# Optimization experiments

Hardware: AMD Instinct MI355X
Metric: run time of the kernel (lower is better)

Reference implementation:

```python
import jax, jax.numpy as jnp
import numpy as np

B, N, D = 512, 101, 128
H = D
NHEADS = 8
HD = H // NHEADS
NSTEPS = 140


def setup_inputs() -> dict:
    key = jax.random.key(0)
    ks = jax.random.split(key, 12)
    enc = jax.random.normal(ks[0], (B, N, D), jnp.float32)
    pool = jax.random.normal(ks[1], (B, H), jnp.float32)
    # CVRP-style demands: depot demand 0, customers in (0, 0.2); capacity normalized to 1.0
    demand = jax.random.uniform(ks[2], (B, N), jnp.float32) * 0.2
    demand = demand.at[:, 0].set(0.0)
    capcity = jnp.ones((B, 1), jnp.float32)
    actions_old = jax.random.randint(ks[3], (B, NSTEPS), 0, N, dtype=jnp.int32)

    def lin(k, fin, fout):
        return (jax.random.normal(k, (fin, fout), jnp.float32) / np.sqrt(fin)).astype(jnp.float32)

    return dict(
        encoder_inputs=enc, pool=pool, actions_old=actions_old,
        capcity=capcity, demand=demand, n_steps=NSTEPS, batch_size=B,
        W_fc=lin(ks[4], H + 1, H),      # Decoder1.fc  (no bias)
        W_fc1=lin(ks[5], H, H),         # Decoder1.fc1
        W_w=lin(ks[6], D, H),           # Attention1.w (cat=1)
        W_k=lin(ks[7], D, H),           # Attention1.k
        W_v=lin(ks[8], D, H),           # Attention1.v
        W_attnfc=lin(ks[9], H, H),      # Attention1.fc
        W_pk=lin(ks[10], D, H),         # ProbAttention.k
    )


def reference(encoder_inputs, pool, actions_old, capcity, demand, n_steps, batch_size,
              W_fc, W_fc1, W_w, W_k, W_v, W_attnfc, W_pk):
    Bs, Nn, Dd = encoder_inputs.shape
    Hh = W_fc.shape[1]
    nh = NHEADS
    hd = Hh // nh
    cap0 = capcity[0, 0]  # torch: capcity[0].item()
    demands = demand
    col = jnp.arange(Nn)

    # context is constant across decode steps -> hoist K/V/pointer-K projections
    Kh = (encoder_inputs @ W_k).reshape(Bs, Nn, nh, hd).transpose(0, 2, 1, 3)  # (B,h,N,hd)
    Vh = (encoder_inputs @ W_v).reshape(Bs, Nn, nh, hd).transpose(0, 2, 1, 3)
    Kp = encoder_inputs @ W_pk  # (B,N,H)

    def update_mask(mask1, dyn_cap, index):
        # mask1: visited nodes (bool). depot masked iff we just arrived at depot.
        go_depot = index == 0
        m1 = jnp.logical_or(mask1, col[None, :] == index[:, None])
        m1 = m1.at[:, 0].set(go_depot)
        mask = jnp.logical_or(m1, demands > dyn_cap)  # dyn_cap (B,1) broadcasts
        # guard: if everything masked (instance finished), allow depot (torch code
        # breaks out of the loop instead; log_p is zeroed by is_done either way)
        all_masked = jnp.all(mask, axis=1)
        mask = mask.at[:, 0].set(jnp.where(all_masked, False, mask[:, 0]))
        return mask, m1

    def update_state(dyn_cap, index):
        cur = jnp.take_along_axis(demands, index[:, None], axis=1)
        dyn = dyn_cap - cur
        return jnp.where((index == 0)[:, None], cap0, dyn)

    mask1_init = jnp.zeros((Bs, Nn), bool)
    idx0 = jnp.zeros((Bs,), jnp.int32)
    mask_init, mask1_init = update_mask(mask1_init, capcity, idx0)  # i == 0 update

    def step(carry, _):
        _input, dyn_cap, mask, mask1, pool_c = carry
        dec = jnp.concatenate([_input, dyn_cap], axis=-1) @ W_fc  # (B,H)
        pool_n = pool_c @ W_fc1                                   # pool re-projected EVERY step (as in torch)
        dec = dec + pool_n
        # --- Attention1 (multi-head glimpse) ---
        Q = (dec @ W_w).reshape(Bs, nh, hd)
        compat = jnp.einsum('bhd,bhnd->bhn', Q, Kh) * (1.0 / np.sqrt(hd))
        u = jnp.where(mask[:, None, :], -jnp.inf, compat)
        sc = jax.nn.softmax(u, axis=-1)
        glimpse = jnp.einsum('bhn,bhnd->bhd', sc, Vh).reshape(Bs, Hh) @ W_attnfc
        # --- ProbAttention (tanh-clipped pointer) ---
        comp2 = jnp.einsum('bh,bnh->bn', glimpse, Kp) * (1.0 / np.sqrt(Hh))
        logits = jnp.where(mask, -jnp.inf, 10.0 * jnp.tanh(comp2))
        logp_all = jax.nn.log_softmax(logits, axis=-1)
        index = jnp.argmax(logp_all, axis=-1)  # greedy decode
        log_p = jnp.take_along_axis(logp_all, index[:, None], axis=1)[:, 0]
        is_done = (jnp.sum(mask1[:, 1:].astype(jnp.int32), axis=1) >= (Nn - 1)).astype(log_p.dtype)
        log_p = log_p * (1.0 - is_done)
        dyn_new = jax.lax.stop_gradient(update_state(dyn_cap, index))  # torch .detach()
        mask_new, mask1_new = update_mask(mask1, dyn_new, index)
        inp_new = jnp.take_along_axis(encoder_inputs, index[:, None, None], axis=1)[:, 0, :]
        return (inp_new, dyn_new, mask_new, mask1_new, pool_n), (index, log_p)

    carry0 = (encoder_inputs[:, 0, :], capcity, mask_init, mask1_init, pool)
    _, (actions, log_ps) = jax.lax.scan(step, carry0, None, length=int(n_steps))
    actions = actions.T            # (B, n_steps)
    log_p = jnp.sum(log_ps, axis=0)  # (B,)
    return actions, log_p
```

## Files before the change

### kernel.cpp

```cpp
#include <hip/hip_runtime.h>
#include <math.h>

#define B_ 512
#define N_ 101
#define H_ 128
#define T_ 140
#define M37 0x1FFFFFFFFFull

#define BAR() asm volatile("s_waitcnt lgkmcnt(0)\n\ts_barrier" ::: "memory")
#define LGKM0() asm volatile("s_waitcnt lgkmcnt(0)" ::: "memory")

template <int CTRL, int RM>
__device__ __forceinline__ float dpp_max_step(float x) {
  int t = __builtin_amdgcn_update_dpp((int)0xFF800000, __float_as_int(x), CTRL, RM, 0xF, false);
  return fmaxf(x, __int_as_float(t));
}
template <int CTRL, int RM>
__device__ __forceinline__ float dpp_add_step(float x) {
  int t = __builtin_amdgcn_update_dpp(0, __float_as_int(x), CTRL, RM, 0xF, false);
  return x + __int_as_float(t);
}
__device__ __forceinline__ float wave_max64(float x) {
  x = dpp_max_step<0x111, 0xF>(x);
  x = dpp_max_step<0x112, 0xF>(x);
  x = dpp_max_step<0x114, 0xF>(x);
  x = dpp_max_step<0x118, 0xF>(x);
  x = dpp_max_step<0x142, 0xA>(x);
  x = dpp_max_step<0x143, 0xC>(x);
  return __int_as_float(__builtin_amdgcn_readlane(__float_as_int(x), 63));
}
__device__ __forceinline__ float wave_sum64(float x) {
  x = dpp_add_step<0x111, 0xF>(x);
  x = dpp_add_step<0x112, 0xF>(x);
  x = dpp_add_step<0x114, 0xF>(x);
  x = dpp_add_step<0x118, 0xF>(x);
  x = dpp_add_step<0x142, 0xA>(x);
  x = dpp_add_step<0x143, 0xC>(x);
  return __int_as_float(__builtin_amdgcn_readlane(__float_as_int(x), 63));
}

__device__ __forceinline__ void gemm_tile_dev(
    const float* A, const float* B, float* C, int cb, int transB, int tid)
{
  int cc = cb * 32 + (tid & 7) * 4;
  int r0 = tid >> 3;
  float4 acc0 = {0,0,0,0}, acc1 = {0,0,0,0}, acc2 = {0,0,0,0}, acc3 = {0,0,0,0};
  for (int k = 0; k < 128; ++k) {
    float4 b4;
    if (!transB) {
      b4 = *(const float4*)(B + k * 128 + cc);
    } else {
      b4.x = B[(cc + 0) * 128 + k];
      b4.y = B[(cc + 1) * 128 + k];
      b4.z = B[(cc + 2) * 128 + k];
      b4.w = B[(cc + 3) * 128 + k];
    }
    float a0 = A[(r0 +  0) * 128 + k];
    float a1 = A[(r0 + 32) * 128 + k];
    float a2 = A[(r0 + 64) * 128 + k];
    float a3 = A[(r0 + 96) * 128 + k];
    acc0.x += a0 * b4.x; acc0.y += a0 * b4.y; acc0.z += a0 * b4.z; acc0.w += a0 * b4.w;
    acc1.x += a1 * b4.x; acc1.y += a1 * b4.y; acc1.z += a1 * b4.z; acc1.w += a1 * b4.w;
    acc2.x += a2 * b4.x; acc2.y += a2 * b4.y; acc2.z += a2 * b4.z; acc2.w += a2 * b4.w;
    acc3.x += a3 * b4.x; acc3.y += a3 * b4.y; acc3.z += a3 * b4.z; acc3.w += a3 * b4.w;
  }
  *(float4*)(C + (r0 +  0) * 128 + cc) = acc0;
  *(float4*)(C + (r0 + 32) * 128 + cc) = acc1;
  *(float4*)(C + (r0 + 64) * 128 + cc) = acc2;
  *(float4*)(C + (r0 + 96) * 128 + cc) = acc3;
}

__global__ __launch_bounds__(256) void stage_a(
    const float* __restrict__ Wfc, const float* __restrict__ Ww,
    const float* __restrict__ Wpk, const float* __restrict__ Wat,
    const float* __restrict__ F,
    float* __restrict__ Wfw, float* __restrict__ Wc, float* __restrict__ wcap,
    float* __restrict__ Mbuf)
{
  int j = blockIdx.x, tid = threadIdx.x;
  if (j < 4)       gemm_tile_dev(Wfc, Ww, Wfw, j, 0, tid);
  else if (j < 8)  gemm_tile_dev(Wpk, Wat, Wc, j - 4, 1, tid);
  else if (j == 8) {
    if (tid < 128) {
      float s = 0.f;
      for (int k = 0; k < 128; ++k) s += Wfc[128 * 128 + k] * Ww[k * 128 + tid];
      wcap[tid] = s;
    }
  } else gemm_tile_dev(F, F, Mbuf + 2ll * 16384, j - 9, 0, tid);
}

__global__ __launch_bounds__(256) void stage_b(
    const float* __restrict__ F, const float* __restrict__ enc,
    const float* __restrict__ Wfw, float* __restrict__ Mbuf,
    float* __restrict__ encW)
{
  int bx = blockIdx.x, tid = threadIdx.x;
  if (bx < 8) {
    int s = (bx >> 2) + 1, cb = bx & 3;
    const float* As = (s == 1) ? F : Mbuf + (long long)s * 16384;
    gemm_tile_dev(As, Mbuf + 2ll * 16384, Mbuf + (long long)(2 + s) * 16384, cb, 0, tid);
  } else {
    int jj = bx - 8, rb = jj >> 2, cb = jj & 3;
    gemm_tile_dev(enc + (long long)rb * 16384, Wfw, encW + (long long)rb * 16384, cb, 0, tid);
  }
}

__global__ __launch_bounds__(256) void chainL(
    const float* __restrict__ F, float* __restrict__ Mbuf, int L)
{
  int bx = blockIdx.x, tid = threadIdx.x;
  int s = (bx >> 2) + 1, cb = bx & 3;
  const float* As = (s == 1) ? F : Mbuf + (long long)s * 16384;
  gemm_tile_dev(As, Mbuf + (long long)L * 16384, Mbuf + (long long)(L + s) * 16384, cb, 0, tid);
}

__global__ __launch_bounds__(256) void stage_n8(
    const float* __restrict__ F, const float* __restrict__ Ww,
    float* __restrict__ Mbuf, float* __restrict__ Abuf)
{
  int bx = blockIdx.x, tid = threadIdx.x;
  if (bx < 48) {
    int s = (bx >> 2) + 1, cb = bx & 3;
    const float* As = (s == 1) ? F : Mbuf + (long long)s * 16384;
    gemm_tile_dev(As, Mbuf + 128ll * 16384, Mbuf + (long long)(128 + s) * 16384, cb, 0, tid);
  } else {
    int jj = bx - 48, t = jj >> 2, cb = jj & 3;
    const float* Ms = (t == 0) ? F : Mbuf + (long long)(t + 1) * 16384;
    gemm_tile_dev(Ms, Ww, Abuf + (long long)t * 16384, cb, 0, tid);
  }
}

__global__ __launch_bounds__(256) void stage_n9(
    const float* __restrict__ Ww, const float* __restrict__ pool,
    float* __restrict__ Mbuf, float* __restrict__ Abuf, float* __restrict__ Qpl)
{
  int bx = blockIdx.x, tid = threadIdx.x;
  if (bx < 52) {
    int t = 127 + (bx >> 2), cb = bx & 3;
    gemm_tile_dev(Mbuf + (long long)(t + 1) * 16384, Ww, Abuf + (long long)t * 16384, cb, 0, tid);
  } else {
    int jj = bx - 52, t = jj >> 4, sub = jj & 15, rb = sub >> 2, cb = sub & 3;
    gemm_tile_dev(pool + (long long)rb * 16384, Abuf + (long long)t * 16384,
                  Qpl + (long long)t * 65536 + (long long)rb * 16384, cb, 0, tid);
  }
}

__global__ __launch_bounds__(256) void stage_n10(
    const float* __restrict__ pool, float* __restrict__ Abuf, float* __restrict__ Qpl)
{
  int bx = blockIdx.x, tid = threadIdx.x;
  int t = 127 + (bx >> 4), sub = bx & 15, rb = sub >> 2, cb = sub & 3;
  gemm_tile_dev(pool + (long long)rb * 16384, Abuf + (long long)t * 16384,
                Qpl + (long long)t * 65536 + (long long)rb * 16384, cb, 0, tid);
}

__device__ __forceinline__ void compat_sm(
    int wave, int lane, int amaxU, float capU,
    unsigned long long msklo, unsigned long long mskhi,
    const float* s_buf, const float* s_wc, const float* s_qp,
    float* s_qs, const float* kreg, float* s_sc)
{
  if (lane < 32) {
    int d = (lane < 16) ? (wave * 16 + lane) : ((wave + 4) * 16 + (lane - 16));
    float qv = s_buf[amaxU * H_ + d] + capU * s_wc[d] + s_qp[d];
    s_qs[wave * 32 + lane] = qv;
  }
  LGKM0();
  const float4* q0 = (const float4*)(s_qs + wave * 32);
  const float4* q1 = (const float4*)(s_qs + wave * 32 + 16);
  float c00 = 0.f, c01 = 0.f, c10 = 0.f, c11 = 0.f;
#pragma unroll
  for (int q = 0; q < 4; ++q) {
    float4 qq = q0[q];
    c00 += qq.x * kreg[q * 4 + 0] + qq.y * kreg[q * 4 + 1]
         + qq.z * kreg[q * 4 + 2] + qq.w * kreg[q * 4 + 3];
    c10 += qq.x * kreg[32 + q * 4 + 0] + qq.y * kreg[32 + q * 4 + 1]
         + qq.z * kreg[32 + q * 4 + 2] + qq.w * kreg[32 + q * 4 + 3];
    float4 qr = q1[q];
    c01 += qr.x * kreg[16 + q * 4 + 0] + qr.y * kreg[16 + q * 4 + 1]
         + qr.z * kreg[16 + q * 4 + 2] + qr.w * kreg[16 + q * 4 + 3];
    c11 += qr.x * kreg[48 + q * 4 + 0] + qr.y * kreg[48 + q * 4 + 1]
         + qr.z * kreg[48 + q * 4 + 2] + qr.w * kreg[48 + q * 4 + 3];
  }
  bool mb0 = (msklo >> lane) & 1ull;
  bool mb1v = (lane < 37) ? ((mskhi >> lane) & 1ull) : true;
  float a0 = mb0 ? -INFINITY : 0.25f * c00;
  float a1 = mb0 ? -INFINITY : 0.25f * c01;
  float b0 = mb1v ? -INFINITY : 0.25f * c10;
  float b1 = mb1v ? -INFINITY : 0.25f * c11;

  float m0  = wave_max64(fmaxf(a0, b0));
  float m1v = wave_max64(fmaxf(a1, b1));
  float ea0 = expf(a0 - m0),  eb0 = (lane < 37) ? expf(b0 - m0)  : 0.f;
  float ea1 = expf(a1 - m1v), eb1 = (lane < 37) ? expf(b1 - m1v) : 0.f;
  float s0 = ea0 + eb0, s1 = ea1 + eb1;
#pragma unroll
  for (int off = 32; off > 0; off >>= 1) {
    s0 += __shfl_xor(s0, off);
    s1 += __shfl_xor(s1, off);
  }
  float* r0 = s_sc + wave * 104;
  float* r1 = s_sc + (wave + 4) * 104;
  r0[lane] = ea0 / s0; r1[lane] = ea1 / s1;
  if (lane < 37) { r0[64 + lane] = eb0 / s0; r1[64 + lane] = eb1 / s1; }
}

__global__ __attribute__((amdgpu_flat_work_group_size(256, 256), amdgpu_waves_per_eu(2, 2)))
void decode_kernel(
    const float* __restrict__ enc,
    const float* __restrict__ Wk,
    const float* __restrict__ Wv,
    const float* __restrict__ Wc,
    const float* __restrict__ encW,
    const float* __restrict__ Qpool,
    const float* __restrict__ wcap,
    const float* __restrict__ capcity,
    const float* __restrict__ demand,
    float* __restrict__ out)
{
  __shared__ __align__(16) float s_buf[N_ * 132];
  __shared__ __align__(16) float s_sc[8 * 104];
  __shared__ __align__(16) float s_part[256];
  __shared__ __align__(16) float s_p2[256];
  __shared__ __align__(16) float s_qs[128];
  __shared__ __align__(16) float s_wc[128];
  __shared__ __align__(16) float s_qp[128];

  const int b    = blockIdx.x;
  const int tid  = threadIdx.x;
  const int lane = tid & 63;
  const int wave = tid >> 6;
  const int an = tid & 127, aj = tid >> 7;
  const int bh2 = (lane >> 4) & 1;
  const int bj2 = (wave + ((lane >= 32) ? 4 : 0)) * 16 + (lane & 15);
  const float invSqrtH = 0.08838834764831845f;

  float cap  = capcity[b];
  float cap0 = capcity[0];
  float dem0 = demand[(long long)b * N_ + lane];
  float dem1 = (lane < 37) ? demand[(long long)b * N_ + 64 + lane] : 0.f;
  float wcr  = (tid < 128) ? wcap[tid] : 0.f;
  float qp0  = (tid < 128) ? Qpool[(long long)b * H_ + tid] : 0.f;

  for (int idx = tid; idx < N_ * 32; idx += 256) {
    int row = idx >> 5, q = idx & 31;
    float4 v = *(const float4*)(enc + ((long long)b * N_ + row) * H_ + q * 4);
    float* d = s_buf + row * 132 + q * 4;
    d[0] = v.x; d[1] = v.y; d[2] = v.z; d[3] = v.w;
  }
  BAR();

  float vreg[51];
#pragma unroll
  for (int q = 0; q < 51; ++q) vreg[q] = 0.f;
  {
    const int base = bh2 * 51;
    for (int i4 = 0; i4 < 32; ++i4) {
      float w0 = Wv[(i4 * 4 + 0) * H_ + bj2];
      float w1 = Wv[(i4 * 4 + 1) * H_ + bj2];
      float w2 = Wv[(i4 * 4 + 2) * H_ + bj2];
      float w3 = Wv[(i4 * 4 + 3) * H_ + bj2];
#pragma unroll
      for (int nl = 0; nl < 51; ++nl) {
        if (base + nl < N_) {
          float4 e = *(const float4*)(s_buf + (base + nl) * 132 + i4 * 4);
          vreg[nl] += e.x * w0 + e.y * w1 + e.z * w2 + e.w * w3;
        }
      }
    }
  }

  float kreg[64];
#pragma unroll
  for (int q = 0; q < 64; ++q) kreg[q] = 0.f;
  {
    const int n0 = lane;
    const int n1c = (lane < 37) ? 64 + lane : 0;
    for (int i = 0; i < 128; ++i) {
      float e0 = s_buf[n0 * 132 + i];
      float e1 = s_buf[n1c * 132 + i];
      const float4* wk0 = (const float4*)(Wk + i * H_ + wave * 16);
      const float4* wk1 = (const float4*)(Wk + i * H_ + (wave + 4) * 16);
#pragma unroll
      for (int q = 0; q < 4; ++q) {
        float4 a = wk0[q];
        kreg[q * 4 + 0] += e0 * a.x; kreg[q * 4 + 1] += e0 * a.y;
        kreg[q * 4 + 2] += e0 * a.z; kreg[q * 4 + 3] += e0 * a.w;
        kreg[32 + q * 4 + 0] += e1 * a.x; kreg[32 + q * 4 + 1] += e1 * a.y;
        kreg[32 + q * 4 + 2] += e1 * a.z; kreg[32 + q * 4 + 3] += e1 * a.w;
        float4 c = wk1[q];
        kreg[16 + q * 4 + 0] += e0 * c.x; kreg[16 + q * 4 + 1] += e0 * c.y;
        kreg[16 + q * 4 + 2] += e0 * c.z; kreg[16 + q * 4 + 3] += e0 * c.w;
        kreg[48 + q * 4 + 0] += e1 * c.x; kreg[48 + q * 4 + 1] += e1 * c.y;
        kreg[48 + q * 4 + 2] += e1 * c.z; kreg[48 + q * 4 + 3] += e1 * c.w;
      }
    }
  }

  float preg[64];
#pragma unroll
  for (int q = 0; q < 64; ++q) preg[q] = 0.f;
  if (an < N_) {
    for (int i = 0; i < 128; ++i) {
      float e = s_buf[an * 132 + i];
      const float4* wc = (const float4*)(Wc + i * H_ + aj * 64);
#pragma unroll
      for (int q = 0; q < 16; ++q) {
        float4 c = wc[q];
        preg[q * 4 + 0] += e * c.x; preg[q * 4 + 1] += e * c.y;
        preg[q * 4 + 2] += e * c.z; preg[q * 4 + 3] += e * c.w;
      }
    }
  }
  BAR();

  for (int idx = tid; idx < N_ * 32; idx += 256) {
    int row = idx >> 5, q = idx & 31;
    float4 v = *(const float4*)(encW + ((long long)b * N_ + row) * H_ + q * 4);
    float* d = s_buf + row * 128 + q * 4;
    d[0] = v.x; d[1] = v.y; d[2] = v.z; d[3] = v.w;
  }
  if (tid < 128) { s_wc[tid] = wcr; s_qp[tid] = qp0; }
  BAR();

  unsigned long long m1lo = 1ull, m1hi = 0ull;
  unsigned long long msklo, mskhi;
  {
    bool p0i = (lane == 0) || (dem0 > cap);
    bool p1i = (lane < 37) ? (dem1 > cap) : true;
    msklo = __ballot(p0i);
    mskhi = __ballot(p1i) & M37;
    if (msklo == ~0ull && mskhi == M37) msklo &= ~1ull;
  }
  float logpAcc = 0.f;
  compat_sm(wave, lane, 0, cap, msklo, mskhi, s_buf, s_wc, s_qp, s_qs, kreg, s_sc);

  for (int t = 0; t < T_; ++t) {
    int tn = (t + 1 < T_) ? (t + 1) : t;
    float qn = (tid < 128) ? Qpool[((long long)tn * B_ + b) * H_ + tid] : 0.f;

    {
      LGKM0();
      const float* srow = s_sc + (bj2 >> 4) * 104;
      float acc = 0.f;
      if (bh2 == 0) {
#pragma unroll
        for (int q = 0; q < 12; ++q) {
          float4 sv = *(const float4*)(srow + q * 4);
          acc += sv.x * vreg[q * 4 + 0] + sv.y * vreg[q * 4 + 1]
               + sv.z * vreg[q * 4 + 2] + sv.w * vreg[q * 4 + 3];
        }
        acc += srow[48] * vreg[48] + srow[49] * vreg[49] + srow[50] * vreg[50];
      } else {
        acc += srow[51] * vreg[0];
#pragma unroll
        for (int q = 0; q < 12; ++q) {
          float4 sv = *(const float4*)(srow + 52 + q * 4);
          acc += sv.x * vreg[1 + q * 4] + sv.y * vreg[2 + q * 4]
               + sv.z * vreg[3 + q * 4] + sv.w * vreg[4 + q * 4];
        }
        acc += srow[100] * vreg[49];
      }
      s_part[bh2 * 128 + bj2] = acc;
    }
    BAR();

    if (an < N_) {
      const float4* p0 = (const float4*)(s_part + aj * 64);
      const float4* p1 = (const float4*)(s_part + 128 + aj * 64);
      float c = 0.f;
#pragma unroll
      for (int q = 0; q < 16; ++q) {
        float4 g0 = p0[q], g1 = p1[q];
        float gx = g0.x + g1.x, gy = g0.y + g1.y, gz = g0.z + g1.z, gw = g0.w + g1.w;
        c += gx * preg[q * 4 + 0] + gy * preg[q * 4 + 1]
           + gz * preg[q * 4 + 2] + gw * preg[q * 4 + 3];
      }
      s_p2[aj * 128 + an] = c;
    }
    if (tid < 128) s_qp[tid] = qn;
    BAR();

    {
      float l0 = -INFINITY, l1 = -INFINITY;
      bool mb0 = (msklo >> lane) & 1ull;
      if (!mb0) l0 = 10.f * tanhf((s_p2[lane] + s_p2[128 + lane]) * invSqrtH);
      if (lane < 37) {
        bool mb1 = (mskhi >> lane) & 1ull;
        if (!mb1) l1 = 10.f * tanhf((s_p2[64 + lane] + s_p2[192 + lane]) * invSqrtH);
      }
      float vmax = wave_max64(fmaxf(l0, l1));
      unsigned long long blo = __ballot(l0 == vmax);
      unsigned long long bhi = __ballot(l1 == vmax);
      int amax = blo ? (__ffsll((long long)blo) - 1)
                     : (64 + __ffsll((long long)bhi) - 1);
      float ss = wave_sum64(__expf(l0 - vmax) + __expf(l1 - vmax));
      logpAcc -= __logf(ss);

      float dlo = __int_as_float(__builtin_amdgcn_readlane(__float_as_int(dem0), amax & 63));
      float dhi = __int_as_float(__builtin_amdgcn_readlane(__float_as_int(dem1), amax & 63));
      float capNew = (amax == 0) ? cap0 : (cap - ((amax < 64) ? dlo : dhi));
      if (amax < 64) m1lo |= (1ull << amax); else m1hi |= (1ull << (amax - 64));
      m1lo = (m1lo & ~1ull) | (unsigned long long)(amax == 0);
      bool doneNew = ((int)__popcll(m1lo & ~1ull) + (int)__popcll(m1hi)) >= (N_ - 1);
      bool p0m = ((m1lo >> lane) & 1ull) || (dem0 > capNew);
      bool p1m = (lane < 37) ? (((m1hi >> lane) & 1ull) || (dem1 > capNew)) : true;
      unsigned long long klo = __ballot(p0m);
      unsigned long long khi = __ballot(p1m) & M37;
      if (klo == ~0ull && khi == M37) klo &= ~1ull;
      msklo = klo; mskhi = khi; cap = capNew;

      if (tid == 0) out[(long long)b * T_ + t] = (float)amax;
      if (doneNew) {
        for (int tt = t + 1 + tid; tt < T_; tt += 256)
          out[(long long)b * T_ + tt] = 0.f;
        break;
      }
      if (t + 1 < T_)
        compat_sm(wave, lane, amax, capNew, msklo, mskhi,
                  s_buf, s_wc, s_qp, s_qs, kreg, s_sc);
    }
  }

  if (tid == 0) out[(long long)B_ * T_ + b] = logpAcc;
}

extern "C" void kernel_launch(void* const* d_in, const int* in_sizes, int n_in,
                              void* d_out, int out_size, void* d_ws, size_t ws_size,
                              hipStream_t stream)
{
  const float* enc   = (const float*)d_in[0];
  const float* pool  = (const float*)d_in[1];
  const float* cap   = (const float*)d_in[3];
  const float* dem   = (const float*)d_in[4];
  const float* W_fc  = (const float*)d_in[7];
  const float* W_fc1 = (const float*)d_in[8];
  const float* W_w   = (const float*)d_in[9];
  const float* W_kk  = (const float*)d_in[10];
  const float* W_vv  = (const float*)d_in[11];
  const float* W_at  = (const float*)d_in[12];
  const float* W_pk  = (const float*)d_in[13];
  float* out = (float*)d_out;
  float* ws  = (float*)d_ws;

  float* Mbuf  = ws;
  float* Abuf  = Mbuf + 141 * 16384;
  float* Qpl   = Abuf + 140 * 16384;
  float* encW  = Qpl + 140 * 512 * 128;
  float* Wfw   = encW + 512 * 101 * 128;
  float* Wc    = Wfw + 16384;
  float* wcapb = Wc + 16384;

  stage_a<<<13, 256, 0, stream>>>(W_fc, W_w, W_pk, W_at, W_fc1, Wfw, Wc, wcapb, Mbuf);
  stage_b<<<1624, 256, 0, stream>>>(W_fc1, enc, Wfw, Mbuf, encW);
  chainL<<<16, 256, 0, stream>>>(W_fc1, Mbuf, 4);
  chainL<<<32, 256, 0, stream>>>(W_fc1, Mbuf, 8);
  chainL<<<64, 256, 0, stream>>>(W_fc1, Mbuf, 16);
  chainL<<<128, 256, 0, stream>>>(W_fc1, Mbuf, 32);
  chainL<<<256, 256, 0, stream>>>(W_fc1, Mbuf, 64);
  stage_n8<<<556, 256, 0, stream>>>(W_fc1, W_w, Mbuf, Abuf);
  stage_n9<<<2084, 256, 0, stream>>>(W_w, pool, Mbuf, Abuf, Qpl);
  stage_n10<<<208, 256, 0, stream>>>(pool, Abuf, Qpl);
  decode_kernel<<<512, 256, 0, stream>>>(enc, W_kk, W_vv, Wc, encW, Qpl, wcapb, cap, dem, out);
}
```

Measured before the change: 1.046 ms.

## Merge precompute stage kernels into one persistent kernel with grid barriers

Replaces the ten separate precompute launches (weight folding, power chain of W_fc1, per-step query projections) with a single persistent kernel of 512 blocks. The blocks walk each stage's tile list in a grid-stride loop and meet at an atomic grid barrier between stages. The aim is to remove per-launch overhead and the tail gaps between dependent stages. The cost is a spin-wait barrier that relies on all 512 blocks being resident at once, one extra memset, and a bounded spin that could break out early and produce wrong results under contention.

```diff
diff --git a/kernel.cpp b/kernel.cpp
--- a/kernel.cpp
+++ b/kernel.cpp
@@ -6,6 +6,7 @@
 #define H_ 128
 #define T_ 140
 #define M37 0x1FFFFFFFFFull
+#define PRE_NBLK 512
 
 #define BAR() asm volatile("s_waitcnt lgkmcnt(0)\n\ts_barrier" ::: "memory")
 #define LGKM0() asm volatile("s_waitcnt lgkmcnt(0)" ::: "memory")
@@ -70,88 +71,105 @@
   *(float4*)(C + (r0 + 96) * 128 + cc) = acc3;
 }
 
-__global__ __launch_bounds__(256) void stage_a(
-    const float* __restrict__ Wfc, const float* __restrict__ Ww,
-    const float* __restrict__ Wpk, const float* __restrict__ Wat,
-    const float* __restrict__ F,
-    float* __restrict__ Wfw, float* __restrict__ Wc, float* __restrict__ wcap,
-    float* __restrict__ Mbuf)
+__device__ __forceinline__ void gsync(int* bar) {
+  __syncthreads();
+  if (threadIdx.x == 0) {
+    __threadfence();
+    int g = __hip_atomic_load(bar + 1, __ATOMIC_RELAXED, __HIP_MEMORY_SCOPE_AGENT);
+    int arrived = __hip_atomic_fetch_add(bar, 1, __ATOMIC_ACQ_REL, __HIP_MEMORY_SCOPE_AGENT);
+    if (arrived == PRE_NBLK - 1) {
+      __hip_atomic_store(bar, 0, __ATOMIC_RELAXED, __HIP_MEMORY_SCOPE_AGENT);
+      __hip_atomic_store(bar + 1, g + 1, __ATOMIC_RELEASE, __HIP_MEMORY_SCOPE_AGENT);
+    } else {
+      int spins = 0;
+      while (__hip_atomic_load(bar + 1, __ATOMIC_ACQUIRE, __HIP_MEMORY_SCOPE_AGENT) == g) {
+        __builtin_amdgcn_s_sleep(8);
+        if (++spins > (1 << 21)) break;
+      }
+    }
+    __threadfence();
+  }
+  __syncthreads();
+}
+
+__global__ __launch_bounds__(256) void precompute_mega(
+    const float* __restrict__ enc, const float* __restrict__ pool,
+    const float* __restrict__ Wfc, const float* __restrict__ F ,
+    const float* __restrict__ Ww,  const float* __restrict__ Wat,
+    const float* __restrict__ Wpk,
+    float* __restrict__ Mbuf, float* __restrict__ Abuf,
+    float* __restrict__ Qpl,  float* __restrict__ encW,
+    float* __restrict__ Wfw,  float* __restrict__ Wc,
+    float* __restrict__ wcapb, int* __restrict__ bar)
 {
-  int j = blockIdx.x, tid = threadIdx.x;
-  if (j < 4)       gemm_tile_dev(Wfc, Ww, Wfw, j, 0, tid);
-  else if (j < 8)  gemm_tile_dev(Wpk, Wat, Wc, j - 4, 1, tid);
-  else if (j == 8) {
-    if (tid < 128) {
-      float s = 0.f;
-      for (int k = 0; k < 128; ++k) s += Wfc[128 * 128 + k] * Ww[k * 128 + tid];
-      wcap[tid] = s;
-    }
-  } else gemm_tile_dev(F, F, Mbuf + 2ll * 16384, j - 9, 0, tid);
-}
-
-__global__ __launch_bounds__(256) void stage_b(
-    const float* __restrict__ F, const float* __restrict__ enc,
-    const float* __restrict__ Wfw, float* __restrict__ Mbuf,
-    float* __restrict__ encW)
-{
-  int bx = blockIdx.x, tid = threadIdx.x;
-  if (bx < 8) {
-    int s = (bx >> 2) + 1, cb = bx & 3;
-    const float* As = (s == 1) ? F : Mbuf + (long long)s * 16384;
-    gemm_tile_dev(As, Mbuf + 2ll * 16384, Mbuf + (long long)(2 + s) * 16384, cb, 0, tid);
-  } else {
-    int jj = bx - 8, rb = jj >> 2, cb = jj & 3;
-    gemm_tile_dev(enc + (long long)rb * 16384, Wfw, encW + (long long)rb * 16384, cb, 0, tid);
-  }
-}
-
-__global__ __launch_bounds__(256) void chainL(
-    const float* __restrict__ F, float* __restrict__ Mbuf, int L)
-{
-  int bx = blockIdx.x, tid = threadIdx.x;
-  int s = (bx >> 2) + 1, cb = bx & 3;
-  const float* As = (s == 1) ? F : Mbuf + (long long)s * 16384;
-  gemm_tile_dev(As, Mbuf + (long long)L * 16384, Mbuf + (long long)(L + s) * 16384, cb, 0, tid);
-}
-
-__global__ __launch_bounds__(256) void stage_n8(
-    const float* __restrict__ F, const float* __restrict__ Ww,
-    float* __restrict__ Mbuf, float* __restrict__ Abuf)
-{
-  int bx = blockIdx.x, tid = threadIdx.x;
-  if (bx < 48) {
-    int s = (bx >> 2) + 1, cb = bx & 3;
-    const float* As = (s == 1) ? F : Mbuf + (long long)s * 16384;
-    gemm_tile_dev(As, Mbuf + 128ll * 16384, Mbuf + (long long)(128 + s) * 16384, cb, 0, tid);
-  } else {
-    int jj = bx - 48, t = jj >> 2, cb = jj & 3;
-    const float* Ms = (t == 0) ? F : Mbuf + (long long)(t + 1) * 16384;
-    gemm_tile_dev(Ms, Ww, Abuf + (long long)t * 16384, cb, 0, tid);
-  }
-}
-
-__global__ __launch_bounds__(256) void stage_n9(
-    const float* __restrict__ Ww, const float* __restrict__ pool,
-    float* __restrict__ Mbuf, float* __restrict__ Abuf, float* __restrict__ Qpl)
-{
-  int bx = blockIdx.x, tid = threadIdx.x;
-  if (bx < 52) {
-    int t = 127 + (bx >> 2), cb = bx & 3;
-    gemm_tile_dev(Mbuf + (long long)(t + 1) * 16384, Ww, Abuf + (long long)t * 16384, cb, 0, tid);
-  } else {
-    int jj = bx - 52, t = jj >> 4, sub = jj & 15, rb = sub >> 2, cb = sub & 3;
+  const int tid = threadIdx.x;
+  const int bx  = blockIdx.x;
+
+  for (int j = bx; j < 13; j += PRE_NBLK) {
+    if (j < 4)       gemm_tile_dev(Wfc, Ww, Wfw, j, 0, tid);
+    else if (j < 8)  gemm_tile_dev(Wpk, Wat, Wc, j - 4, 1, tid);
+    else if (j == 8) {
+      if (tid < 128) {
+        float s = 0.f;
+        for (int k = 0; k < 128; ++k) s += Wfc[128 * 128 + k] * Ww[k * 128 + tid];
+        wcapb[tid] = s;
+      }
+    } else gemm_tile_dev(F, F, Mbuf + 2ll * 16384, j - 9, 0, tid);
+  }
+  gsync(bar);
+
+  for (int j = bx; j < 1624; j += PRE_NBLK) {
+    if (j < 8) {
+      int s = (j >> 2) + 1, cb = j & 3;
+      const float* As = (s == 1) ? F : Mbuf + (long long)s * 16384;
+      gemm_tile_dev(As, Mbuf + 2ll * 16384, Mbuf + (long long)(2 + s) * 16384, cb, 0, tid);
+    } else {
+      int jj = j - 8, rb = jj >> 2, cb = jj & 3;
+      gemm_tile_dev(enc + (long long)rb * 16384, Wfw, encW + (long long)rb * 16384, cb, 0, tid);
+    }
+  }
+  gsync(bar);
+
+  for (int L = 4; L <= 64; L <<= 1) {
+    int cjobs = 4 * L;
+    for (int j = bx; j < cjobs; j += PRE_NBLK) {
+      int s = (j >> 2) + 1, cb = j & 3;
+      const float* As = (s == 1) ? F : Mbuf + (long long)s * 16384;
+      gemm_tile_dev(As, Mbuf + (long long)L * 16384, Mbuf + (long long)(L + s) * 16384, cb, 0, tid);
+    }
+    gsync(bar);
+  }
+
+  for (int j = bx; j < 556; j += PRE_NBLK) {
+    if (j < 48) {
+      int s = (j >> 2) + 1, cb = j & 3;
+      const float* As = (s == 1) ? F : Mbuf + (long long)s * 16384;
+      gemm_tile_dev(As, Mbuf + 128ll * 16384, Mbuf + (long long)(128 + s) * 16384, cb, 0, tid);
+    } else {
+      int jj = j - 48, t = jj >> 2, cb = jj & 3;
+      const float* Ms = (t == 0) ? F : Mbuf + (long long)(t + 1) * 16384;
+      gemm_tile_dev(Ms, Ww, Abuf + (long long)t * 16384, cb, 0, tid);
+    }
+  }
+  gsync(bar);
+
+  for (int j = bx; j < 2084; j += PRE_NBLK) {
+    if (j < 52) {
+      int t = 127 + (j >> 2), cb = j & 3;
+      gemm_tile_dev(Mbuf + (long long)(t + 1) * 16384, Ww, Abuf + (long long)t * 16384, cb, 0, tid);
+    } else {
+      int jj = j - 52, t = jj >> 4, sub = jj & 15, rb = sub >> 2, cb = sub & 3;
+      gemm_tile_dev(pool + (long long)rb * 16384, Abuf + (long long)t * 16384,
+                    Qpl + (long long)t * 65536 + (long long)rb * 16384, cb, 0, tid);
+    }
+  }
+  gsync(bar);
+
+  for (int j = bx; j < 208; j += PRE_NBLK) {
+    int t = 127 + (j >> 4), sub = j & 15, rb = sub >> 2, cb = sub & 3;
     gemm_tile_dev(pool + (long long)rb * 16384, Abuf + (long long)t * 16384,
                   Qpl + (long long)t * 65536 + (long long)rb * 16384, cb, 0, tid);
   }
-}
-
-__global__ __launch_bounds__(256) void stage_n10(
-    const float* __restrict__ pool, float* __restrict__ Abuf, float* __restrict__ Qpl)
-{
-  int bx = blockIdx.x, tid = threadIdx.x;
-  int t = 127 + (bx >> 4), sub = bx & 15, rb = sub >> 2, cb = sub & 3;
-  gemm_tile_dev(pool + (long long)rb * 16384, Abuf + (long long)t * 16384,
-                Qpl + (long long)t * 65536 + (long long)rb * 16384, cb, 0, tid);
 }
 
 __device__ __forceinline__ void compat_sm(
@@ -450,16 +468,11 @@
   float* Wfw   = encW + 512 * 101 * 128;
   float* Wc    = Wfw + 16384;
   float* wcapb = Wc + 16384;
-
-  stage_a<<<13, 256, 0, stream>>>(W_fc, W_w, W_pk, W_at, W_fc1, Wfw, Wc, wcapb, Mbuf);
-  stage_b<<<1624, 256, 0, stream>>>(W_fc1, enc, Wfw, Mbuf, encW);
-  chainL<<<16, 256, 0, stream>>>(W_fc1, Mbuf, 4);
-  chainL<<<32, 256, 0, stream>>>(W_fc1, Mbuf, 8);
-  chainL<<<64, 256, 0, stream>>>(W_fc1, Mbuf, 16);
-  chainL<<<128, 256, 0, stream>>>(W_fc1, Mbuf, 32);
-  chainL<<<256, 256, 0, stream>>>(W_fc1, Mbuf, 64);
-  stage_n8<<<556, 256, 0, stream>>>(W_fc1, W_w, Mbuf, Abuf);
-  stage_n9<<<2084, 256, 0, stream>>>(W_w, pool, Mbuf, Abuf, Qpl);
-  stage_n10<<<208, 256, 0, stream>>>(pool, Abuf, Qpl);
+  int*   bar   = (int*)(wcapb + 128);
+
+  hipMemsetAsync(bar, 0, 2 * sizeof(int), stream);
+  precompute_mega<<<PRE_NBLK, 256, 0, stream>>>(
+      enc, pool, W_fc, W_fc1, W_w, W_at, W_pk,
+      Mbuf, Abuf, Qpl, encW, Wfw, Wc, wcapb, bar);
   decode_kernel<<<512, 256, 0, stream>>>(enc, W_kk, W_vv, Wc, encW, Qpl, wcapb, cap, dem, out);
 }
```

Result: slower. 2.379 ms (+127.5%).
